# Kernel optimization log

Hardware: AMD Instinct MI355X
Metric: run time of the kernel (lower is better)

Reference implementation:

```python
import jax, jax.numpy as jnp
import numpy as np
from jax import lax

B, L, S, D = 2, 8, 512, 256


def setup_inputs() -> dict:
    key = jax.random.key(0)
    ks = jax.random.split(key, 12)
    s = 1.0 / np.sqrt(D)
    return {
        "features": jax.random.normal(ks[0], (B, L, S, D), jnp.float32),
        "source_features": jax.random.normal(ks[1], (B, S, D), jnp.float32),
        "target_features": jax.random.normal(ks[2], (B, S, D), jnp.float32),
        # GRU params (torch layout: [3D, D] with gate order r, z, n)
        "W_ih": jax.random.uniform(ks[3], (3 * D, D), jnp.float32, -s, s),
        "W_hh": jax.random.uniform(ks[4], (3 * D, D), jnp.float32, -s, s),
        "b_ih": jax.random.uniform(ks[5], (3 * D,), jnp.float32, -s, s),
        "b_hh": jax.random.uniform(ks[6], (3 * D,), jnp.float32, -s, s),
        # causal_predictor: Linear(2D, D) -> ReLU -> Linear(D, D) -> Sigmoid
        "W1": jax.random.uniform(ks[7], (D, 2 * D), jnp.float32, -s, s),
        "b1": jax.random.uniform(ks[8], (D,), jnp.float32, -s, s),
        "W2": jax.random.uniform(ks[9], (D, D), jnp.float32, -s, s),
        "b2": jax.random.uniform(ks[10], (D,), jnp.float32, -s, s),
    }


def _gru(x, W_ih, W_hh, b_ih, b_hh):
    # x: [N, T, D] batch-first; returns all hidden states [N, T, D]
    N, T, d = x.shape
    gx = jnp.einsum('ntd,gd->ntg', x, W_ih) + b_ih  # [N, T, 3D]

    def step(h, gx_t):
        gh = h @ W_hh.T + b_hh
        r = jax.nn.sigmoid(gx_t[:, :d] + gh[:, :d])
        z = jax.nn.sigmoid(gx_t[:, d:2 * d] + gh[:, d:2 * d])
        n = jnp.tanh(gx_t[:, 2 * d:] + r * gh[:, 2 * d:])
        h_new = (1.0 - z) * n + z * h
        return h_new, h_new

    h0 = jnp.zeros((N, d), x.dtype)
    _, outs = lax.scan(step, h0, jnp.swapaxes(gx, 0, 1))  # [T, N, D]
    return jnp.swapaxes(outs, 0, 1)


def reference(features, source_features, target_features,
              W_ih, W_hh, b_ih, b_hh, W1, b1, W2, b2):
    b, l, s, d = features.shape
    fdim = jnp.float32(d)

    # --- track_feature_evolution, vectorized over seq positions ---
    # per-position GRU over the layer axis == one GRU over a B*S batch
    x = jnp.transpose(features, (0, 2, 1, 3)).reshape(b * s, l, d)
    evolution_out = _gru(x, W_ih, W_hh, b_ih, b_hh).reshape(b, s, l, d)

    prev = features[:, :-1]            # [B, L-1, S, D]
    nxt = features[:, 1:]
    eps = jnp.float32(1e-8)
    na = jnp.maximum(jnp.linalg.norm(prev, axis=-1), eps)
    nb = jnp.maximum(jnp.linalg.norm(nxt, axis=-1), eps)
    stability = (jnp.sum(prev * nxt, axis=-1) / (na * nb)).mean(axis=0)  # [L-1, S]

    act = jnp.sum((features > 0.1).astype(jnp.float32), axis=-1)  # [B, L, S]
    emergence = (act[:, 1:] - act[:, :-1]).mean(axis=0) / fdim    # [L-1, S]
    decay = (act[:, :-1] - act[:, 1:]).mean(axis=0) / fdim        # [L-1, S]

    # --- compute_causal_strength ---
    # combined[b,s,i,:D] = source[b,s,:]; combined[b,s,i,D+k] = target[b,s,i] (all k)
    # first Linear(2D->D) therefore splits into:  source @ W1a^T  +  target_i * sum_k W1b[:,k]
    W1a = W1[:, :d]                     # [D, D]
    wb = jnp.sum(W1[:, d:], axis=1)     # [D]
    A = jnp.einsum('bsd,od->bso', source_features, W1a) + b1  # [B, S, D]
    h = A[:, :, None, :] + target_features[:, :, :, None] * wb  # [B, S, D(i), D(o)]
    h = jax.nn.relu(h)
    out2 = jax.nn.sigmoid(jnp.einsum('bsio,po->bsip', h, W2) + b2)  # [B, S, D, D]
    causal_matrix = out2.mean(axis=(0, 1))  # [D, D]

    return stability, emergence, decay, causal_matrix, evolution_out
```

## Files before the change

kernel.cpp:

```cpp
#include <hip/hip_runtime.h>
#include <hip/hip_bf16.h>
#include <stdint.h>

typedef unsigned short u16;
typedef __bf16 v8bf __attribute__((ext_vector_type(8)));
typedef float f32x4 __attribute__((ext_vector_type(4)));

#define WS_WB    0u
#define WS_WIHB  4096u
#define WS_WHHB  397312u
#define WS_W2B   790528u
#define WS_A     921600u
#define WS_GX    2097152u
#define WS_PART  27262976u

#define OUT_STAB   0
#define OUT_EMER   3584
#define OUT_DECAY  7168
#define OUT_CAUSAL 10752
#define OUT_EVO    76288

__device__ __forceinline__ u16 f2bfu(float f){
    union { float f; uint32_t u; } v; v.f = f;
    uint32_t u = v.u;
    return (u16)((u + 0x7fffu + ((u >> 16) & 1u)) >> 16);
}
__device__ __forceinline__ float sigmoidf_fast(float x){
    float e = __builtin_amdgcn_exp2f(-1.4426950408889634f * x);
    return __builtin_amdgcn_rcpf(1.0f + e);
}
__device__ __forceinline__ float tanhf_fast(float x){
    float e = __builtin_amdgcn_exp2f(-2.8853900817779268f * x);
    return __builtin_amdgcn_rcpf(1.0f + e) * 2.0f - 1.0f;
}
__device__ __forceinline__ f32x4 mfma16(v8bf a, v8bf b, f32x4 c){
    return __builtin_amdgcn_mfma_f32_16x16x32_bf16(a, b, c, 0, 0, 0);
}
__device__ __forceinline__ v8bf cvt8(const float* p){
    float4 a = *(const float4*)p;
    float4 b = *(const float4*)(p + 4);
    v8bf r;
    r[0] = (__bf16)a.x; r[1] = (__bf16)a.y; r[2] = (__bf16)a.z; r[3] = (__bf16)a.w;
    r[4] = (__bf16)b.x; r[5] = (__bf16)b.y; r[6] = (__bf16)b.z; r[7] = (__bf16)b.w;
    return r;
}

__global__ __launch_bounds__(256) void k_pre(
        const float* __restrict__ feat, const float* __restrict__ src,
        const float* __restrict__ Wih,  const float* __restrict__ Whh,
        const float* __restrict__ W1,   const float* __restrict__ b1,
        const float* __restrict__ W2,
        u16* __restrict__ wihb, u16* __restrict__ whhb, u16* __restrict__ w2b,
        float* __restrict__ wb, float* __restrict__ A, float* __restrict__ out){
    const int bid = blockIdx.x, tid = threadIdx.x;
    if (bid < 64){
        const int bs0 = bid * 16;
        const int lane = tid & 63, w = tid >> 6;
        const int l15 = lane & 15, quad = lane >> 4;
        v8bf xa[8];
        for (int k = 0; k < 8; k++)
            xa[k] = cvt8(&src[(bs0 + l15) * 256 + k * 32 + quad * 8]);
        f32x4 acc[4];
        for (int nt = 0; nt < 4; nt++) acc[nt] = (f32x4){0.f, 0.f, 0.f, 0.f};
        for (int k = 0; k < 8; k++){
            int d0 = k * 32 + quad * 8;
            for (int nt = 0; nt < 4; nt++){
                int o = w * 64 + nt * 16 + l15;
                v8bf bfr = cvt8(&W1[o * 512 + d0]);
                acc[nt] = mfma16(xa[k], bfr, acc[nt]);
            }
        }
        for (int nt = 0; nt < 4; nt++){
            int o = w * 64 + nt * 16 + l15;
            float bb = b1[o];
            for (int r = 0; r < 4; r++)
                A[(bs0 + quad * 4 + r) * 256 + o] = acc[nt][r] + bb;
        }
    } else if (bid < 960){
        const int pair = (bid - 64) * 4 + (tid >> 6);
        const int l = pair >> 9, s = pair & 511;
        const int lane = tid & 63;
        float stab = 0.f, emer = 0.f;
        for (int b = 0; b < 2; b++){
            const float* p = feat + ((size_t)((b * 8 + l) * 512 + s)) * 256;
            const float* n = feat + ((size_t)((b * 8 + l + 1) * 512 + s)) * 256;
            float4 pv = *(const float4*)(p + lane * 4);
            float4 nv = *(const float4*)(n + lane * 4);
            float dot = pv.x * nv.x + pv.y * nv.y + pv.z * nv.z + pv.w * nv.w;
            float na2 = pv.x * pv.x + pv.y * pv.y + pv.z * pv.z + pv.w * pv.w;
            float nb2 = nv.x * nv.x + nv.y * nv.y + nv.z * nv.z + nv.w * nv.w;
            float ap = ((pv.x > 0.1f) ? 1.f : 0.f) + ((pv.y > 0.1f) ? 1.f : 0.f)
                     + ((pv.z > 0.1f) ? 1.f : 0.f) + ((pv.w > 0.1f) ? 1.f : 0.f);
            float an = ((nv.x > 0.1f) ? 1.f : 0.f) + ((nv.y > 0.1f) ? 1.f : 0.f)
                     + ((nv.z > 0.1f) ? 1.f : 0.f) + ((nv.w > 0.1f) ? 1.f : 0.f);
            for (int off = 32; off > 0; off >>= 1){
                dot += __shfl_xor(dot, off);
                na2 += __shfl_xor(na2, off);
                nb2 += __shfl_xor(nb2, off);
                ap  += __shfl_xor(ap,  off);
                an  += __shfl_xor(an,  off);
            }
            float na = fmaxf(__builtin_sqrtf(na2), 1e-8f);
            float nb = fmaxf(__builtin_sqrtf(nb2), 1e-8f);
            stab += dot / (na * nb);
            emer += (an - ap);
        }
        if (lane == 0){
            int o = l * 512 + s;
            float e = emer * 0.5f * (1.0f / 256.0f);
            out[OUT_STAB  + o] = stab * 0.5f;
            out[OUT_EMER  + o] = e;
            out[OUT_DECAY + o] = -e;
        }
    } else {
        int idx8 = (bid - 960) * 256 + tid;
        if (idx8 < 57344){
            const float* srcp;
            u16* dstp;
            if (idx8 < 24576){ srcp = Wih + idx8 * 8;             dstp = wihb + idx8 * 8; }
            else if (idx8 < 49152){ int i = idx8 - 24576; srcp = Whh + i * 8; dstp = whhb + i * 8; }
            else { int i = idx8 - 49152; srcp = W2 + i * 8; dstp = w2b + i * 8; }
            float4 a = *(const float4*)srcp;
            float4 b = *(const float4*)(srcp + 4);
            union { u16 h[8]; uint4 v; } pk;
            pk.h[0] = f2bfu(a.x); pk.h[1] = f2bfu(a.y);
            pk.h[2] = f2bfu(a.z); pk.h[3] = f2bfu(a.w);
            pk.h[4] = f2bfu(b.x); pk.h[5] = f2bfu(b.y);
            pk.h[6] = f2bfu(b.z); pk.h[7] = f2bfu(b.w);
            *(uint4*)dstp = pk.v;
        } else if (idx8 < 57600){
            int o = idx8 - 57344;
            float s = 0.f;
            const float4* p = (const float4*)&W1[o * 512 + 256];
            for (int j = 0; j < 64; j++){
                float4 v = p[j];
                s += v.x + v.y + v.z + v.w;
            }
            wb[o] = s;
        }
    }
}

__global__ __launch_bounds__(256, 2) void k_mid(
        const float* __restrict__ feat, const u16* __restrict__ wihb,
        const float* __restrict__ bih,  float* __restrict__ gxws,
        const float* __restrict__ Aws,  const float* __restrict__ wbws,
        const u16* __restrict__ w2b,    const float* __restrict__ tgt,
        const float* __restrict__ b2,   float* __restrict__ part){
    __shared__ __align__(16) unsigned char smem[71680];
    const int tid = threadIdx.x, lane = tid & 63, w = tid >> 6;
    const int l15 = lane & 15, quad = lane >> 4;

    if (blockIdx.x < 384){
        const int mb = blockIdx.x / 6, nb = blockIdx.x % 6;
        u16* blds = (u16*)smem;

        {
            int r = tid >> 1, half = tid & 1;
            const uint4* gsrc = (const uint4*)&wihb[(nb * 128 + r) * 256 + half * 128];
            uint4* ldst = (uint4*)&blds[r * 264 + half * 128];
            for (int j = 0; j < 16; j++) ldst[j] = gsrc[j];
        }

        v8bf af[2][8];
        for (int mt = 0; mt < 2; mt++){
            int r = mb * 128 + w * 32 + mt * 16 + l15;
            int n = r >> 3, t = r & 7;
            int b = n >> 9, s = n & 511;
            const float* xp = feat + ((size_t)((b * 8 + t) * 512 + s)) * 256;
            for (int kk = 0; kk < 8; kk++)
                af[mt][kk] = cvt8(xp + kk * 32 + quad * 8);
        }
        __syncthreads();

        f32x4 acc[2][8];
        for (int mt = 0; mt < 2; mt++) for (int nt = 0; nt < 8; nt++)
            acc[mt][nt] = (f32x4){0.f, 0.f, 0.f, 0.f};
        for (int kk = 0; kk < 8; kk++){
            int k0 = kk * 32 + quad * 8;
            for (int nt = 0; nt < 8; nt++){
                v8bf bf = *(const v8bf*)&blds[(nt * 16 + l15) * 264 + k0];
                acc[0][nt] = mfma16(af[0][kk], bf, acc[0][nt]);
                acc[1][nt] = mfma16(af[1][kk], bf, acc[1][nt]);
            }
        }
        for (int nt = 0; nt < 8; nt++){
            int g = nb * 128 + nt * 16 + l15;
            float bias = bih[g];
            for (int mt = 0; mt < 2; mt++)
                for (int rr = 0; rr < 4; rr++){
                    int row = mb * 128 + w * 32 + mt * 16 + quad * 4 + rr;
                    gxws[(size_t)row * 768 + g] = acc[mt][nt][rr] + bias;
                }
        }
        return;
    }

    const int bidc = blockIdx.x - 384;
    const int chunk = bidc >> 2, q = bidc & 3;
    const int i0 = (q & 1) * 128, p0 = (q >> 1) * 128;

    u16*  w2s  = (u16*)smem;
    float* a_db = (float*)(smem + 67584);
    float* t_db = (float*)(smem + 69632);
    float* wb_s = (float*)(smem + 70656);

    {
        int r = tid >> 1, half = tid & 1;
        const uint4* gsrc = (const uint4*)&w2b[(p0 + r) * 256 + half * 128];
        uint4* ldst = (uint4*)&w2s[r * 264 + half * 128];
        for (int j = 0; j < 16; j++) ldst[j] = gsrc[j];
    }
    wb_s[tid] = wbws[tid];
    a_db[tid] = Aws[chunk * 8 * 256 + tid];
    if (tid < 128) t_db[tid] = tgt[(chunk * 8) * 256 + i0 + tid];

    float bb[8];
    for (int nt = 0; nt < 8; nt++) bb[nt] = b2[p0 + nt * 16 + l15];

    f32x4 sig[2][8];
    for (int mt = 0; mt < 2; mt++) for (int nt = 0; nt < 8; nt++)
        sig[mt][nt] = (f32x4){0.f, 0.f, 0.f, 0.f};

    for (int ss = 0; ss < 8; ss++){
        __syncthreads();
        if (ss < 7){
            int nb = (ss + 1) & 1;
            a_db[nb * 256 + tid] = Aws[(chunk * 8 + ss + 1) * 256 + tid];
            if (tid < 128) t_db[nb * 128 + tid] = tgt[(chunk * 8 + ss + 1) * 256 + i0 + tid];
        }
        const int cb = ss & 1;
        float tv0 = t_db[cb * 128 + w * 32 + l15];
        float tv1 = t_db[cb * 128 + w * 32 + 16 + l15];

        f32x4 acc[2][8];
        for (int mt = 0; mt < 2; mt++) for (int nt = 0; nt < 8; nt++)
            acc[mt][nt] = (f32x4){0.f, 0.f, 0.f, 0.f};

        for (int k = 0; k < 8; k++){
            const int o0 = k * 32 + quad * 8;
            float4 a0  = *(const float4*)&a_db[cb * 256 + o0];
            float4 a1  = *(const float4*)&a_db[cb * 256 + o0 + 4];
            float4 w0  = *(const float4*)&wb_s[o0];
            float4 w1v = *(const float4*)&wb_s[o0 + 4];
            v8bf afr0, afr1;
            {
                float t = tv0;
                afr0[0] = (__bf16)fmaxf(fmaf(t, w0.x,  a0.x), 0.f);
                afr0[1] = (__bf16)fmaxf(fmaf(t, w0.y,  a0.y), 0.f);
                afr0[2] = (__bf16)fmaxf(fmaf(t, w0.z,  a0.z), 0.f);
                afr0[3] = (__bf16)fmaxf(fmaf(t, w0.w,  a0.w), 0.f);
                afr0[4] = (__bf16)fmaxf(fmaf(t, w1v.x, a1.x), 0.f);
                afr0[5] = (__bf16)fmaxf(fmaf(t, w1v.y, a1.y), 0.f);
                afr0[6] = (__bf16)fmaxf(fmaf(t, w1v.z, a1.z), 0.f);
                afr0[7] = (__bf16)fmaxf(fmaf(t, w1v.w, a1.w), 0.f);
            }
            {
                float t = tv1;
                afr1[0] = (__bf16)fmaxf(fmaf(t, w0.x,  a0.x), 0.f);
                afr1[1] = (__bf16)fmaxf(fmaf(t, w0.y,  a0.y), 0.f);
                afr1[2] = (__bf16)fmaxf(fmaf(t, w0.z,  a0.z), 0.f);
                afr1[3] = (__bf16)fmaxf(fmaf(t, w0.w,  a0.w), 0.f);
                afr1[4] = (__bf16)fmaxf(fmaf(t, w1v.x, a1.x), 0.f);
                afr1[5] = (__bf16)fmaxf(fmaf(t, w1v.y, a1.y), 0.f);
                afr1[6] = (__bf16)fmaxf(fmaf(t, w1v.z, a1.z), 0.f);
                afr1[7] = (__bf16)fmaxf(fmaf(t, w1v.w, a1.w), 0.f);
            }
            for (int nt = 0; nt < 8; nt++){
                v8bf bfr = *(const v8bf*)&w2s[(nt * 16 + l15) * 264 + o0];
                acc[0][nt] = mfma16(afr0, bfr, acc[0][nt]);
                acc[1][nt] = mfma16(afr1, bfr, acc[1][nt]);
            }
        }
        for (int mt = 0; mt < 2; mt++)
            for (int nt = 0; nt < 8; nt++)
                for (int r = 0; r < 4; r++)
                    sig[mt][nt][r] += sigmoidf_fast(acc[mt][nt][r] + bb[nt]);
    }

    float* pp = part + (size_t)chunk * 65536;
    for (int mt = 0; mt < 2; mt++)
        for (int r = 0; r < 4; r++){
            int i = i0 + w * 32 + mt * 16 + quad * 4 + r;
            for (int nt = 0; nt < 8; nt++){
                int p = p0 + nt * 16 + l15;
                pp[i * 256 + p] = sig[mt][nt][r];
            }
        }
}

__global__ __launch_bounds__(512) void k_final(
        const float* __restrict__ gxws, const u16* __restrict__ whhb,
        const float* __restrict__ bhh, const float* __restrict__ part,
        float* __restrict__ out){
    if (blockIdx.x >= 64){
        const int idx = (blockIdx.x - 64) * 512 + threadIdx.x;
        float s = 0.f;
        for (int c = 0; c < 128; c++)
            s += part[(size_t)c * 65536 + idx];
        out[OUT_CAUSAL + idx] = s * (1.0f / 1024.0f);
        return;
    }
    const int n0 = blockIdx.x * 16;
    const int tid = threadIdx.x, lane = tid & 63, wv = tid >> 6;
    const int l15 = lane & 15, quad = lane >> 4;
    const int g0 = wv * 96;

    __shared__ float h_lds[16 * 260];
    __shared__ float g_lds[16 * 776];

    v8bf wreg[3][8];
    for (int nt = 0; nt < 3; nt++)
        for (int k = 0; k < 8; k++)
            wreg[nt][k] = *(const v8bf*)&whhb[(g0 + nt * 16 + l15) * 256 + k * 32 + quad * 8];

    float bias[6];
    for (int nt = 0; nt < 6; nt++) bias[nt] = bhh[g0 + nt * 16 + l15];

    for (int e = tid; e < 16 * 260; e += 512) h_lds[e] = 0.f;

    const int seq = tid >> 5, d0 = (tid & 31) * 8;
    const float* gxbase = gxws + (size_t)(n0 + seq) * 8 * 768 + d0;
    float* evobase = out + OUT_EVO + (size_t)(n0 + seq) * 8 * 256 + d0;
    __syncthreads();

    for (int t = 0; t < 8; t++){
        v8bf ha[8];
        for (int k = 0; k < 8; k++)
            ha[k] = cvt8(&h_lds[l15 * 260 + k * 32 + quad * 8]);
        f32x4 acc[6];
        for (int nt = 0; nt < 6; nt++) acc[nt] = (f32x4){0.f, 0.f, 0.f, 0.f};
        for (int k = 0; k < 8; k++){
            int dk = k * 32 + quad * 8;
            acc[0] = mfma16(ha[k], wreg[0][k], acc[0]);
            acc[1] = mfma16(ha[k], wreg[1][k], acc[1]);
            acc[2] = mfma16(ha[k], wreg[2][k], acc[2]);
            for (int nt = 3; nt < 6; nt++){
                v8bf bf = *(const v8bf*)&whhb[(g0 + nt * 16 + l15) * 256 + dk];
                acc[nt] = mfma16(ha[k], bf, acc[nt]);
            }
        }
        for (int nt = 0; nt < 6; nt++){
            int g = g0 + nt * 16 + l15;
            for (int rr = 0; rr < 4; rr++)
                g_lds[(quad * 4 + rr) * 776 + g] = acc[nt][rr] + bias[nt];
        }
        const float* gxp = gxbase + (size_t)t * 768;
        float4 x0a = *(const float4*)(gxp);
        float4 x0b = *(const float4*)(gxp + 4);
        float4 x1a = *(const float4*)(gxp + 256);
        float4 x1b = *(const float4*)(gxp + 260);
        float4 x2a = *(const float4*)(gxp + 512);
        float4 x2b = *(const float4*)(gxp + 516);
        __syncthreads();
        {
            const float* gh = &g_lds[seq * 776];
            float* hp = &h_lds[seq * 260 + d0];
            float4 g0a = *(const float4*)&gh[d0];
            float4 g0b = *(const float4*)&gh[d0 + 4];
            float4 g1a = *(const float4*)&gh[256 + d0];
            float4 g1b = *(const float4*)&gh[260 + d0];
            float4 g2a = *(const float4*)&gh[512 + d0];
            float4 g2b = *(const float4*)&gh[516 + d0];
            float4 h0 = *(const float4*)hp;
            float4 h1 = *(const float4*)(hp + 4);
            float gxr[8] = {x0a.x, x0a.y, x0a.z, x0a.w, x0b.x, x0b.y, x0b.z, x0b.w};
            float gxz[8] = {x1a.x, x1a.y, x1a.z, x1a.w, x1b.x, x1b.y, x1b.z, x1b.w};
            float gxn[8] = {x2a.x, x2a.y, x2a.z, x2a.w, x2b.x, x2b.y, x2b.z, x2b.w};
            float ghr[8] = {g0a.x, g0a.y, g0a.z, g0a.w, g0b.x, g0b.y, g0b.z, g0b.w};
            float ghz[8] = {g1a.x, g1a.y, g1a.z, g1a.w, g1b.x, g1b.y, g1b.z, g1b.w};
            float ghn[8] = {g2a.x, g2a.y, g2a.z, g2a.w, g2b.x, g2b.y, g2b.z, g2b.w};
            float hold[8] = {h0.x, h0.y, h0.z, h0.w, h1.x, h1.y, h1.z, h1.w};
            float hn[8];
            #pragma unroll
            for (int j = 0; j < 8; j++){
                float r  = sigmoidf_fast(gxr[j] + ghr[j]);
                float z  = sigmoidf_fast(gxz[j] + ghz[j]);
                float nn = tanhf_fast(fmaf(r, ghn[j], gxn[j]));
                hn[j] = (1.f - z) * nn + z * hold[j];
            }
            float4 v0 = {hn[0], hn[1], hn[2], hn[3]};
            float4 v1 = {hn[4], hn[5], hn[6], hn[7]};
            *(float4*)hp       = v0;
            *(float4*)(hp + 4) = v1;
            float* ep = evobase + (size_t)t * 256;
            *(float4*)ep       = v0;
            *(float4*)(ep + 4) = v1;
        }
        __syncthreads();
    }
}

extern "C" void kernel_launch(void* const* d_in, const int* in_sizes, int n_in,
                              void* d_out, int out_size, void* d_ws, size_t ws_size,
                              hipStream_t stream){
    const float* feat = (const float*)d_in[0];
    const float* src  = (const float*)d_in[1];
    const float* tgt  = (const float*)d_in[2];
    const float* Wih  = (const float*)d_in[3];
    const float* Whh  = (const float*)d_in[4];
    const float* bih  = (const float*)d_in[5];
    const float* bhh  = (const float*)d_in[6];
    const float* W1   = (const float*)d_in[7];
    const float* b1   = (const float*)d_in[8];
    const float* W2   = (const float*)d_in[9];
    const float* b2   = (const float*)d_in[10];
    float* out = (float*)d_out;
    char* ws = (char*)d_ws;

    float* wb   = (float*)(ws + WS_WB);
    u16*   wihb = (u16*)(ws + WS_WIHB);
    u16*   whhb = (u16*)(ws + WS_WHHB);
    u16*   w2b  = (u16*)(ws + WS_W2B);
    float* Aws  = (float*)(ws + WS_A);
    float* gxws = (float*)(ws + WS_GX);
    float* part = (float*)(ws + WS_PART);

    k_pre  <<<1185, 256, 0, stream>>>(feat, src, Wih, Whh, W1, b1, W2,
                                      wihb, whhb, w2b, wb, Aws, out);
    k_mid  <<<896,  256, 0, stream>>>(feat, wihb, bih, gxws,
                                      Aws, wb, w2b, tgt, b2, part);
    k_final<<<192,  512, 0, stream>>>(gxws, whhb, bhh, part, out);
}
```

Baseline: 222.5 us.

## Fuse GRU gate math into MFMA epilogue and interleave k_mid block roles

The GRU recurrence kernel now gives each wave all three gates (r, z, n) for the same 32 hidden dims. The gate nonlinearities are computed straight from the MFMA accumulators, which removes the g_lds staging buffer and one barrier per step. Hidden state is double-buffered in LDS. k_mid interleaves GEMM blocks and causal blocks in a 3:4 pattern so both kinds of work run concurrently across CUs, and the bf16 conversion and ReLU code is vectorised. The tradeoff is that gx loads and evolution stores become scalar and strided, which may reduce coalescing.

```diff
diff --git a/kernel.cpp b/kernel.cpp
--- a/kernel.cpp
+++ b/kernel.cpp
@@ -5,6 +5,7 @@
 typedef unsigned short u16;
 typedef __bf16 v8bf __attribute__((ext_vector_type(8)));
 typedef float f32x4 __attribute__((ext_vector_type(4)));
+typedef float v8f  __attribute__((ext_vector_type(8)));
 
 #define WS_WB    0u
 #define WS_WIHB  4096u
@@ -39,10 +40,8 @@
 __device__ __forceinline__ v8bf cvt8(const float* p){
     float4 a = *(const float4*)p;
     float4 b = *(const float4*)(p + 4);
-    v8bf r;
-    r[0] = (__bf16)a.x; r[1] = (__bf16)a.y; r[2] = (__bf16)a.z; r[3] = (__bf16)a.w;
-    r[4] = (__bf16)b.x; r[5] = (__bf16)b.y; r[6] = (__bf16)b.z; r[7] = (__bf16)b.w;
-    return r;
+    v8f v = {a.x, a.y, a.z, a.w, b.x, b.y, b.z, b.w};
+    return __builtin_convertvector(v, v8bf);
 }
 
 __global__ __launch_bounds__(256) void k_pre(
@@ -150,9 +149,11 @@
     __shared__ __align__(16) unsigned char smem[71680];
     const int tid = threadIdx.x, lane = tid & 63, w = tid >> 6;
     const int l15 = lane & 15, quad = lane >> 4;
-
-    if (blockIdx.x < 384){
-        const int mb = blockIdx.x / 6, nb = blockIdx.x % 6;
+    const int grp = blockIdx.x / 7, q7 = blockIdx.x % 7;
+
+    if (q7 < 3){
+        const int gid = grp * 3 + q7;
+        const int mb = gid / 6, nb = gid % 6;
         u16* blds = (u16*)smem;
 
         {
@@ -196,7 +197,7 @@
         return;
     }
 
-    const int bidc = blockIdx.x - 384;
+    const int bidc = grp * 4 + (q7 - 3);
     const int chunk = bidc >> 2, q = bidc & 3;
     const int i0 = (q & 1) * 128, p0 = (q >> 1) * 128;
 
@@ -221,6 +222,8 @@
     f32x4 sig[2][8];
     for (int mt = 0; mt < 2; mt++) for (int nt = 0; nt < 8; nt++)
         sig[mt][nt] = (f32x4){0.f, 0.f, 0.f, 0.f};
+
+    const v8f z8 = {0.f, 0.f, 0.f, 0.f, 0.f, 0.f, 0.f, 0.f};
 
     for (int ss = 0; ss < 8; ss++){
         __syncthreads();
@@ -243,29 +246,12 @@
             float4 a1  = *(const float4*)&a_db[cb * 256 + o0 + 4];
             float4 w0  = *(const float4*)&wb_s[o0];
             float4 w1v = *(const float4*)&wb_s[o0 + 4];
-            v8bf afr0, afr1;
-            {
-                float t = tv0;
-                afr0[0] = (__bf16)fmaxf(fmaf(t, w0.x,  a0.x), 0.f);
-                afr0[1] = (__bf16)fmaxf(fmaf(t, w0.y,  a0.y), 0.f);
-                afr0[2] = (__bf16)fmaxf(fmaf(t, w0.z,  a0.z), 0.f);
-                afr0[3] = (__bf16)fmaxf(fmaf(t, w0.w,  a0.w), 0.f);
-                afr0[4] = (__bf16)fmaxf(fmaf(t, w1v.x, a1.x), 0.f);
-                afr0[5] = (__bf16)fmaxf(fmaf(t, w1v.y, a1.y), 0.f);
-                afr0[6] = (__bf16)fmaxf(fmaf(t, w1v.z, a1.z), 0.f);
-                afr0[7] = (__bf16)fmaxf(fmaf(t, w1v.w, a1.w), 0.f);
-            }
-            {
-                float t = tv1;
-                afr1[0] = (__bf16)fmaxf(fmaf(t, w0.x,  a0.x), 0.f);
-                afr1[1] = (__bf16)fmaxf(fmaf(t, w0.y,  a0.y), 0.f);
-                afr1[2] = (__bf16)fmaxf(fmaf(t, w0.z,  a0.z), 0.f);
-                afr1[3] = (__bf16)fmaxf(fmaf(t, w0.w,  a0.w), 0.f);
-                afr1[4] = (__bf16)fmaxf(fmaf(t, w1v.x, a1.x), 0.f);
-                afr1[5] = (__bf16)fmaxf(fmaf(t, w1v.y, a1.y), 0.f);
-                afr1[6] = (__bf16)fmaxf(fmaf(t, w1v.z, a1.z), 0.f);
-                afr1[7] = (__bf16)fmaxf(fmaf(t, w1v.w, a1.w), 0.f);
-            }
+            v8f a8 = {a0.x, a0.y, a0.z, a0.w, a1.x, a1.y, a1.z, a1.w};
+            v8f w8 = {w0.x, w0.y, w0.z, w0.w, w1v.x, w1v.y, w1v.z, w1v.w};
+            v8f h0v = __builtin_elementwise_max(a8 + tv0 * w8, z8);
+            v8f h1v = __builtin_elementwise_max(a8 + tv1 * w8, z8);
+            v8bf afr0 = __builtin_convertvector(h0v, v8bf);
+            v8bf afr1 = __builtin_convertvector(h1v, v8bf);
             for (int nt = 0; nt < 8; nt++){
                 v8bf bfr = *(const v8bf*)&w2s[(nt * 16 + l15) * 264 + o0];
                 acc[0][nt] = mfma16(afr0, bfr, acc[0][nt]);
@@ -304,88 +290,58 @@
     const int n0 = blockIdx.x * 16;
     const int tid = threadIdx.x, lane = tid & 63, wv = tid >> 6;
     const int l15 = lane & 15, quad = lane >> 4;
-    const int g0 = wv * 96;
-
-    __shared__ float h_lds[16 * 260];
-    __shared__ float g_lds[16 * 776];
+    const int D0 = wv * 32;
+
+    __shared__ float h_lds[2][16 * 260];
+
+    const int gt[6] = {D0, D0 + 16, 256 + D0, 256 + D0 + 16, 512 + D0, 512 + D0 + 16};
 
     v8bf wreg[3][8];
-    for (int nt = 0; nt < 3; nt++)
+    for (int j = 0; j < 3; j++)
         for (int k = 0; k < 8; k++)
-            wreg[nt][k] = *(const v8bf*)&whhb[(g0 + nt * 16 + l15) * 256 + k * 32 + quad * 8];
+            wreg[j][k] = *(const v8bf*)&whhb[(gt[j] + l15) * 256 + k * 32 + quad * 8];
 
     float bias[6];
-    for (int nt = 0; nt < 6; nt++) bias[nt] = bhh[g0 + nt * 16 + l15];
-
-    for (int e = tid; e < 16 * 260; e += 512) h_lds[e] = 0.f;
-
-    const int seq = tid >> 5, d0 = (tid & 31) * 8;
-    const float* gxbase = gxws + (size_t)(n0 + seq) * 8 * 768 + d0;
-    float* evobase = out + OUT_EVO + (size_t)(n0 + seq) * 8 * 256 + d0;
+    for (int j = 0; j < 6; j++) bias[j] = bhh[gt[j] + l15];
+
+    for (int e = tid; e < 16 * 260; e += 512) h_lds[0][e] = 0.f;
     __syncthreads();
 
     for (int t = 0; t < 8; t++){
+        const int cur = t & 1, nxt = cur ^ 1;
+        float gxv[6][4];
+        for (int rr = 0; rr < 4; rr++){
+            const float* gp = gxws + ((size_t)(n0 + quad * 4 + rr) * 8 + t) * 768;
+            for (int j = 0; j < 6; j++)
+                gxv[j][rr] = gp[gt[j] + l15];
+        }
         v8bf ha[8];
         for (int k = 0; k < 8; k++)
-            ha[k] = cvt8(&h_lds[l15 * 260 + k * 32 + quad * 8]);
+            ha[k] = cvt8(&h_lds[cur][l15 * 260 + k * 32 + quad * 8]);
         f32x4 acc[6];
-        for (int nt = 0; nt < 6; nt++) acc[nt] = (f32x4){0.f, 0.f, 0.f, 0.f};
+        for (int j = 0; j < 6; j++) acc[j] = (f32x4){0.f, 0.f, 0.f, 0.f};
         for (int k = 0; k < 8; k++){
             int dk = k * 32 + quad * 8;
             acc[0] = mfma16(ha[k], wreg[0][k], acc[0]);
             acc[1] = mfma16(ha[k], wreg[1][k], acc[1]);
             acc[2] = mfma16(ha[k], wreg[2][k], acc[2]);
-            for (int nt = 3; nt < 6; nt++){
-                v8bf bf = *(const v8bf*)&whhb[(g0 + nt * 16 + l15) * 256 + dk];
-                acc[nt] = mfma16(ha[k], bf, acc[nt]);
-            }
-        }
-        for (int nt = 0; nt < 6; nt++){
-            int g = g0 + nt * 16 + l15;
-            for (int rr = 0; rr < 4; rr++)
-                g_lds[(quad * 4 + rr) * 776 + g] = acc[nt][rr] + bias[nt];
-        }
-        const float* gxp = gxbase + (size_t)t * 768;
-        float4 x0a = *(const float4*)(gxp);
-        float4 x0b = *(const float4*)(gxp + 4);
-        float4 x1a = *(const float4*)(gxp + 256);
-        float4 x1b = *(const float4*)(gxp + 260);
-        float4 x2a = *(const float4*)(gxp + 512);
-        float4 x2b = *(const float4*)(gxp + 516);
-        __syncthreads();
-        {
-            const float* gh = &g_lds[seq * 776];
-            float* hp = &h_lds[seq * 260 + d0];
-            float4 g0a = *(const float4*)&gh[d0];
-            float4 g0b = *(const float4*)&gh[d0 + 4];
-            float4 g1a = *(const float4*)&gh[256 + d0];
-            float4 g1b = *(const float4*)&gh[260 + d0];
-            float4 g2a = *(const float4*)&gh[512 + d0];
-            float4 g2b = *(const float4*)&gh[516 + d0];
-            float4 h0 = *(const float4*)hp;
-            float4 h1 = *(const float4*)(hp + 4);
-            float gxr[8] = {x0a.x, x0a.y, x0a.z, x0a.w, x0b.x, x0b.y, x0b.z, x0b.w};
-            float gxz[8] = {x1a.x, x1a.y, x1a.z, x1a.w, x1b.x, x1b.y, x1b.z, x1b.w};
-            float gxn[8] = {x2a.x, x2a.y, x2a.z, x2a.w, x2b.x, x2b.y, x2b.z, x2b.w};
-            float ghr[8] = {g0a.x, g0a.y, g0a.z, g0a.w, g0b.x, g0b.y, g0b.z, g0b.w};
-            float ghz[8] = {g1a.x, g1a.y, g1a.z, g1a.w, g1b.x, g1b.y, g1b.z, g1b.w};
-            float ghn[8] = {g2a.x, g2a.y, g2a.z, g2a.w, g2b.x, g2b.y, g2b.z, g2b.w};
-            float hold[8] = {h0.x, h0.y, h0.z, h0.w, h1.x, h1.y, h1.z, h1.w};
-            float hn[8];
-            #pragma unroll
-            for (int j = 0; j < 8; j++){
-                float r  = sigmoidf_fast(gxr[j] + ghr[j]);
-                float z  = sigmoidf_fast(gxz[j] + ghz[j]);
-                float nn = tanhf_fast(fmaf(r, ghn[j], gxn[j]));
-                hn[j] = (1.f - z) * nn + z * hold[j];
-            }
-            float4 v0 = {hn[0], hn[1], hn[2], hn[3]};
-            float4 v1 = {hn[4], hn[5], hn[6], hn[7]};
-            *(float4*)hp       = v0;
-            *(float4*)(hp + 4) = v1;
-            float* ep = evobase + (size_t)t * 256;
-            *(float4*)ep       = v0;
-            *(float4*)(ep + 4) = v1;
+            for (int j = 3; j < 6; j++){
+                v8bf bf = *(const v8bf*)&whhb[(gt[j] + l15) * 256 + dk];
+                acc[j] = mfma16(ha[k], bf, acc[j]);
+            }
+        }
+        for (int c = 0; c < 2; c++){
+            const int d = D0 + c * 16 + l15;
+            for (int rr = 0; rr < 4; rr++){
+                const int seq = quad * 4 + rr;
+                float r  = sigmoidf_fast(gxv[c][rr]     + acc[c][rr]     + bias[c]);
+                float z  = sigmoidf_fast(gxv[2 + c][rr] + acc[2 + c][rr] + bias[2 + c]);
+                float nn = tanhf_fast(fmaf(r, acc[4 + c][rr] + bias[4 + c], gxv[4 + c][rr]));
+                float hold = h_lds[cur][seq * 260 + d];
+                float hnew = (1.f - z) * nn + z * hold;
+                h_lds[nxt][seq * 260 + d] = hnew;
+                out[OUT_EVO + ((size_t)(n0 + seq) * 8 + t) * 256 + d] = hnew;
+            }
         }
         __syncthreads();
     }
```

Result: slower. 248.7 us (+11.8%).
